# Kernel optimization log

Hardware: AMD Instinct MI355X
Metric: run time of the kernel (lower is better)

The kernel has to match this reference:

```python
import jax, jax.numpy as jnp
import numpy as np

L = 16          # num_sites
CHI_MAX = 64    # max bond dimension
VOCAB = 128000
TRUNC_EVERY = 10
DT = jnp.float32


def _mps_add(A, B):
    """Direct sum of two MPS (block-diagonal on bonds, boundaries concatenated)."""
    out = []
    for s in range(L):
        a, b = A[s], B[s]
        cla, d, cra = a.shape
        clb, _, crb = b.shape
        if s == 0:
            out.append(jnp.concatenate([a, b], axis=2))          # [1,d,cra+crb]
        elif s == L - 1:
            out.append(jnp.concatenate([a, b], axis=0))          # [cla+clb,d,1]
        else:
            t = jnp.zeros((cla + clb, d, cra + crb), a.dtype)
            t = t.at[:cla, :, :cra].set(a).at[cla:, :, cra:].set(b)
            out.append(t)
    return out


def _truncate(T, chi_max):
    """Left-to-right SVD sweep truncating every bond to <= chi_max."""
    T = list(T)
    for s in range(L - 1):
        cl, d, cr = T[s].shape
        U, S, Vh = jnp.linalg.svd(T[s].reshape(cl * d, cr), full_matrices=False)
        k = min(chi_max, int(S.shape[0]))
        T[s] = U[:, :k].reshape(cl, d, k)
        carry = S[:k, None] * Vh[:k]                              # [k, cr]
        T[s + 1] = jnp.einsum('kl,ldr->kdr', carry, T[s + 1])
    return T


def _forward(cores_hidden, cores_input, head_w, head_b, init_ctx, toks):
    # D=1 MPO core -> per-site 2x2 matrix acting on the physical index
    Wh = cores_hidden[:, 0, :, :, 0]   # [L,2,2]
    Wi = cores_input[:, 0, :, :, 0]    # [L,2,2]
    e0 = jnp.array([1.0, 0.0], DT).reshape(1, 2, 1)
    e1 = jnp.array([0.0, 1.0], DT).reshape(1, 2, 1)
    ctx = [init_ctx[s] for s in range(L)]
    for t, tok in enumerate(toks, start=1):
        bits = [(tok >> i) & 1 for i in range(L)]
        emb = [e1 if b else e0 for b in reversed(bits)]
        # h_{t+1} = W_hidden @ h_t  (+)  W_input @ embed(token)
        h = [jnp.einsum('ij,ljr->lir', Wh[s], ctx[s]) for s in range(L)]
        x = [jnp.einsum('ij,ljr->lir', Wi[s], emb[s]) for s in range(L)]
        ctx = _mps_add(h, x)
        if t % TRUNC_EVERY == 0 and ctx[0].shape[2] > CHI_MAX:
            ctx = _truncate(ctx, CHI_MAX)
    # predict(): mean of middle site over (left bond, phys) -> feature vector
    vec = ctx[L // 2].mean(axis=(0, 1))
    c = vec.shape[0]
    vec = jnp.pad(vec, (0, CHI_MAX - c)) if c < CHI_MAX else vec[:CHI_MAX]
    return head_w @ vec + head_b


def setup_inputs() -> dict:
    key = jax.random.key(0)
    k1, k2, k3, k4, k5, k6 = jax.random.split(key, 6)
    eye = jnp.eye(2, dtype=DT)
    cores_hidden = (0.02 * jax.random.normal(k1, (L, 1, 2, 2, 1), DT)).at[:, 0, :, :, 0].add(eye)
    cores_input = (0.02 * jax.random.normal(k2, (L, 1, 2, 2, 1), DT)).at[:, 0, :, :, 0].add(eye)
    head_w = jax.random.normal(k3, (VOCAB, CHI_MAX), DT) / jnp.sqrt(jnp.float32(CHI_MAX))
    head_b = 0.02 * jax.random.normal(k4, (VOCAB,), DT)
    init_ctx = jax.random.normal(k5, (L, 1, 2, 1), DT)
    token_ids = jax.random.randint(k6, (100,), 0, 65536, dtype=jnp.int32)
    return {"cores_hidden": cores_hidden, "cores_input": cores_input,
            "head_w": head_w, "head_b": head_b,
            "init_ctx": init_ctx, "token_ids": token_ids}


def reference(cores_hidden, cores_input, head_w, head_b, init_ctx, token_ids):
    toks = [int(t) for t in np.asarray(token_ids)]
    return _forward(cores_hidden, cores_input, head_w, head_b, init_ctx, toks)
```

## Files before the change

kernel.cpp:

```cpp
#include <hip/hip_runtime.h>

typedef double rl;
#define NT 256
#define NSV 71
#define LDA 128
#define LDV 72
#define SML 25
#define VOCAB 128000
#define LP 27
#define PB 129

#define EPS32 1.1920928955078125e-7
#define UNFL32 1.17549435e-38

#define O_CAR   0
#define O_COLS  4608
#define O_VEC   4800
#define O_MA    5120
#define O_MBLG  14208
#define O_MU    23552
#define O_MQ    32768
#define O_MVT   41984
#define O_SUB   47168
#define O_SVTB  52352
// ... 210 lines not shown
    for(; i<len; ++i) row[(size_t)ld*(1+i)] -= w*(v[(size_t)vstride*i]*scl);
  }
}

__device__ void bdsqr_wave(int n, rl* d, rl* e, int ncvt, int nru, LeafCtx* lc, int lane){
  if(n>1){
    rl eps=EPS32, unfl=UNFL32;
    rl tolmul=fmax(10.0,fmin(100.0,pow(eps,-0.125)));
    rl tol=tolmul*eps;
    rl thresh=0.0;
    int mm=n-1, oldll=-2, oldm=-2, idir=0, iter=0, maxit=6*n*n;
    if(lane==0){
      rl sminoa=fabs(d[0]);
      if(sminoa!=0.0){
        rl mu=sminoa;
        for(int i=1;i<n;++i){ mu=fabs(d[i])*(mu/(mu+fabs(e[i-1]))); sminoa=fmin(sminoa,mu); if(sminoa==0.0)break; }
      }
      sminoa=sminoa/sqrt((rl)n);
      thresh=fmax(tol*sminoa,(rl)(6*n*n)*unfl);
    }
    while(true){
      if(lane==0){
        int act=0, p_lo=0, p_cnt=0, p_fwd=1, p_mm=0;
        while(mm>0){
          if(iter>maxit) break;
          rl smax=fabs(d[mm]), smin=smax;
          int ll=-1;
          for(int lll=mm-1;lll>=0;--lll){
            rl abss=fabs(d[lll]), abse=fabs(e[lll]);
            if(abse<=thresh){ ll=lll; break; }
            smin=fmin(smin,abss);
            smax=fmax(smax,fmax(abss,abse));
          }
          if(ll==mm-1){ e[ll]=0.0; mm=mm-1; continue; }
          if(ll>=0) e[ll]=0.0;
          int lo=ll+1;
          if(mm==lo+1){
            rl sigmn,sigmx,sinr,cosr,sinl,cosl;
            dlasv2(d[lo],e[lo],d[mm],&sigmn,&sigmx,&sinr,&cosr,&sinl,&cosl);
            d[lo]=sigmx; d[mm]=sigmn; e[lo]=0.0;
            lc->sc[0]=cosr; lc->sc[1]=sinr; lc->sc[2]=cosl; lc->sc[3]=sinl;
            act=2; p_lo=lo; p_mm=mm;
            mm-=2;
            break;
          }
          if(lo>oldm || mm<oldll) idir=(fabs(d[lo])>=fabs(d[mm]))?1:2;
          rl sminl=0.0; int conv=0;
          if(idir==1){
            if(fabs(e[mm-1])<=tol*fabs(d[mm])){ e[mm-1]=0.0; conv=1; }
            if(!conv){
              rl mu=fabs(d[lo]); sminl=mu;
              for(int lll=lo;lll<mm;++lll){
                if(fabs(e[lll])<=tol*mu){ e[lll]=0.0; conv=1; break; }
                mu=fabs(d[lll+1])*(mu/(mu+fabs(e[lll])));
                sminl=fmin(sminl,mu);
              }
            }
          } else {
            if(fabs(e[lo])<=tol*fabs(d[lo])){ e[lo]=0.0; conv=1; }
            if(!conv){
              rl mu=fabs(d[mm]); sminl=mu;
              for(int lll=mm-1;lll>=lo;--lll){
                if(fabs(e[lll])<=tol*mu){ e[lll]=0.0; conv=1; break; }
                mu=fabs(d[lll])*(mu/(mu+fabs(e[lll])));
                sminl=fmin(sminl,mu);
              }
            }
          }
          if(conv) continue;
          oldll=lo; oldm=mm;
          rl shift=0.0, rr_;
          if(!((rl)n*tol*(sminl/smax) <= fmax(eps, 0.01*tol))){
            rl sll;
            if(idir==1){ sll=fabs(d[lo]); dlas2(d[mm-1],e[mm-1],d[mm],&shift,&rr_); }
            else { sll=fabs(d[mm]); dlas2(d[lo],e[lo],d[lo+1],&shift,&rr_); }
            if(sll>0.0){ rl q=shift/sll; if(q*q<eps) shift=0.0; }
          }
          iter += mm-lo;
          int cnt=mm-lo;
          if(shift==0.0){
            if(idir==1){
              rl cs=1.0, oldcs=1.0, sn=0.0, oldsn=0.0, r;
              for(int i=lo;i<mm;++i){
                dlartg(d[i]*cs,e[i],&cs,&sn,&r);
                if(i>lo) e[i-1]=oldsn*r;
                dlartg(oldcs*r, d[i+1]*sn, &oldcs,&oldsn,&d[i]);
                lc->b1[i-lo]=cs; lc->b2[i-lo]=sn; lc->b3[i-lo]=oldcs; lc->b4[i-lo]=oldsn;
              }
              rl h=d[mm]*cs; d[mm]=h*oldcs; e[mm-1]=h*oldsn;
              p_fwd=1;
              if(fabs(e[mm-1])<=thresh) e[mm-1]=0.0;
            } else {
              rl cs=1.0, oldcs=1.0, sn=0.0, oldsn=0.0, r;
              for(int i=mm;i>lo;--i){
                dlartg(d[i]*cs,e[i-1],&cs,&sn,&r);
                if(i<mm) e[i]=oldsn*r;
                dlartg(oldcs*r,d[i-1]*sn,&oldcs,&oldsn,&d[i]);
                int j=i-lo-1;
                lc->b1[j]=oldcs; lc->b2[j]=-oldsn; lc->b3[j]=cs; lc->b4[j]=-sn;
              }
              rl h=d[lo]*cs; d[lo]=h*oldcs; e[lo]=h*oldsn;
              p_fwd=0;
              if(fabs(e[lo])<=thresh) e[lo]=0.0;
            }
          } else {
            if(idir==1){
              rl f2=(fabs(d[lo])-shift)*(d_sign(1.0,d[lo])+shift/d[lo]);
              rl g2=e[lo], r, cosr,sinr,cosl,sinl;
              for(int i=lo;i<mm;++i){
                dlartg(f2,g2,&cosr,&sinr,&r);
                if(i>lo) e[i-1]=r;
                f2=cosr*d[i]+sinr*e[i];
                e[i]=cosr*e[i]-sinr*d[i];
                g2=sinr*d[i+1];
                d[i+1]=cosr*d[i+1];
                dlartg(f2,g2,&cosl,&sinl,&r);
                d[i]=r;
                f2=cosl*e[i]+sinl*d[i+1];
                d[i+1]=cosl*d[i+1]-sinl*e[i];
                if(i<mm-1){ g2=sinl*e[i+1]; e[i+1]=cosl*e[i+1]; }
                lc->b1[i-lo]=cosr; lc->b2[i-lo]=sinr; lc->b3[i-lo]=cosl; lc->b4[i-lo]=sinl;
              }
              e[mm-1]=f2;
              p_fwd=1;
              if(fabs(e[mm-1])<=thresh) e[mm-1]=0.0;
            } else {
              rl f2=(fabs(d[mm])-shift)*(d_sign(1.0,d[mm])+shift/d[mm]);
              rl g2=e[mm-1], r, cosr,sinr,cosl,sinl;
              for(int i=mm;i>lo;--i){
                dlartg(f2,g2,&cosr,&sinr,&r);
                if(i<mm) e[i]=r;
                f2=cosr*d[i]+sinr*e[i-1];
                e[i-1]=cosr*e[i-1]-sinr*d[i];
                g2=sinr*d[i-1];
                d[i-1]=cosr*d[i-1];
                dlartg(f2,g2,&cosl,&sinl,&r);
                d[i]=r;
                f2=cosl*e[i-1]+sinl*d[i-1];
                d[i-1]=cosl*d[i-1]-sinl*e[i-1];
                if(i>lo+1){ g2=sinl*e[i-2]; e[i-2]=cosl*e[i-2]; }
                int j=i-lo-1;
                lc->b1[j]=cosl; lc->b2[j]=-sinl; lc->b3[j]=cosr; lc->b4[j]=-sinr;
              }
              e[lo]=f2;
              p_fwd=0;
              if(fabs(e[lo])<=thresh) e[lo]=0.0;
            }
          }
          act=1; p_lo=lo; p_cnt=cnt;
          break;
        }
        lc->si[7]=act; lc->si[8]=p_lo; lc->si[9]=p_cnt; lc->si[10]=p_fwd; lc->si[11]=p_mm;
      }
      wsync();
      int act=lc->si[7];
      if(act==0) break;
      if(act==1){
        int lo=lc->si[8], cnt=lc->si[9], fwd=lc->si[10];
        if(lane<ncvt){
          int k=lane;
          if(fwd){
            rl cur = lc->LVT[lo*LP+k];
            for(int j=0;j<cnt;++j){
              rl c=lc->b1[j], s=lc->b2[j];
              rl t = lc->LVT[(lo+j+1)*LP+k];
              lc->LVT[(lo+j)*LP+k] = s*t + c*cur;
              cur = c*t - s*cur;
            }
            lc->LVT[(lo+cnt)*LP+k] = cur;
          } else {
            rl tcar = lc->LVT[(lo+cnt)*LP+k];
            for(int j=cnt-1;j>=0;--j){
              rl c=lc->b1[j], s=lc->b2[j];
              rl low = lc->LVT[(lo+j)*LP+k];
              lc->LVT[(lo+j+1)*LP+k] = c*tcar - s*low;
              tcar = s*tcar + c*low;
            }
            lc->LVT[lo*LP+k] = tcar;
          }
        } else if(lane<ncvt+nru){
          int r2=lane-ncvt;
          if(fwd){
            rl cur = lc->LU[r2*LP+lo];
            for(int j=0;j<cnt;++j){
              rl c=lc->b3[j], s=lc->b4[j];
              rl t = lc->LU[r2*LP+(lo+j+1)];
              lc->LU[r2*LP+(lo+j)] = s*t + c*cur;
              cur = c*t - s*cur;
            }
            lc->LU[r2*LP+(lo+cnt)] = cur;
          } else {
            rl tcar = lc->LU[r2*LP+(lo+cnt)];
            for(int j=cnt-1;j>=0;--j){
              rl c=lc->b3[j], s=lc->b4[j];
              rl low = lc->LU[r2*LP+(lo+j)];
              lc->LU[r2*LP+(lo+j+1)] = c*tcar - s*low;
              tcar = s*tcar + c*low;
            }
            lc->LU[r2*LP+lo] = tcar;
          }
        }
      } else {
        int lo=lc->si[8], m2=lc->si[11];
        rl cosr=lc->sc[0], sinr=lc->sc[1], cosl=lc->sc[2], sinl=lc->sc[3];
        if(lane<ncvt){
          rl x=lc->LVT[lo*LP+lane], y=lc->LVT[m2*LP+lane];
          lc->LVT[lo*LP+lane]=cosr*x+sinr*y; lc->LVT[m2*LP+lane]=cosr*y-sinr*x;
        } else if(lane<ncvt+nru){
          int r2=lane-ncvt;
          rl x=lc->LU[r2*LP+lo], y=lc->LU[r2*LP+m2];
          lc->LU[r2*LP+lo]=cosl*x+sinl*y; lc->LU[r2*LP+m2]=cosl*y-sinl*x;
        }
      }
      wsync();
    }
  }
  if(lane==0){
    for(int i=0;i<n;++i){ lc->ic[i]=(d[i]<0.0)?1:0; if(d[i]<0.0) d[i]=-d[i]; }
    int nsw=0;
    for(int i=0;i<n-1;++i){
      int isub=0; rl smin=d[0];
      for(int j=1;j<n-i;++j){ if(d[j]<=smin){ isub=j; smin=d[j]; } }
      int tgt=n-1-i;
      if(isub!=tgt){
        d[isub]=d[tgt]; d[tgt]=smin;
        lc->ia[nsw]=isub; lc->ib[nsw]=tgt; ++nsw;
      }
    }
    lc->si[7]=nsw;
  }
  wsync();
  int nsw=lc->si[7];
  if(lane<ncvt){
    for(int i=0;i<n;++i) if(lc->ic[i]) lc->LVT[i*LP+lane]=-lc->LVT[i*LP+lane];
    for(int w2=0;w2<nsw;++w2){
      int a=lc->ia[w2], b=lc->ib[w2];
      rl t=lc->LVT[a*LP+lane]; lc->LVT[a*LP+lane]=lc->LVT[b*LP+lane]; lc->LVT[b*LP+lane]=t;
    }
  } else if(lane<ncvt+nru){
    int r2=lane-ncvt;
    for(int w2=0;w2<nsw;++w2){
      int a=lc->ia[w2], b=lc->ib[w2];
      rl t=lc->LU[r2*LP+a]; lc->LU[r2*LP+a]=lc->LU[r2*LP+b]; lc->LU[r2*LP+b]=t;
    }
  }
  wsync();
}

__device__ void leaf_exec(int f, int n, int sqre, int wantU, LeafCtx* lc, Sh* sh, int lane){
  rl* SVTB = g_ws + O_SVTB; rl* SUB = g_ws + O_SUB;
  int np = n + sqre;
  for(int w=lane; w<np*np; w+=64){ int r2=w/np, c=w-r2*np; lc->LVT[r2*LP+c]=SVTB[(f+r2)+(size_t)LDV*(f+c)]; }
  if(wantU) for(int w=lane; w<n*n; w+=64){ int r2=w/n, c=w-r2*n; lc->LU[r2*LP+c]=SUB[(f+r2)+(size_t)LDV*(f+c)]; }
  wsync();
  if(sqre==1){
    if(lane==0){
      rl cs,snv,rv; rl* dd=sh->d+f; rl* ee=sh->e+f;
      for(int i=0;i<n;++i){
        dlartg(dd[i],ee[i],&cs,&snv,&rv);
        dd[i]=rv;
        if(i<n-1){ ee[i]=snv*dd[i+1]; dd[i+1]=cs*dd[i+1]; }
        else ee[i]=0.0;
        lc->b1[i]=cs; lc->b2[i]=snv;
      }
    }
    wsync();
    if(lane<np){
      rl cur = lc->LVT[0*LP+lane];
      for(int j=0;j<n;++j){
        rl cj=lc->b1[j], sj=lc->b2[j];
        rl t=lc->LVT[(j+1)*LP+lane];
        lc->LVT[j*LP+lane] = sj*t + cj*cur;
        cur = cj*t - sj*cur;
      }
      lc->LVT[n*LP+lane] = cur;
    }
    wsync();
    if(lane==0){
      rl cs,snv,rv; rl* dd=sh->d+f; rl* ee=sh->e+f;
      for(int i=0;i<n-1;++i){
        dlartg(dd[i],ee[i],&cs,&snv,&rv);
        dd[i]=rv; ee[i]=snv*dd[i+1]; dd[i+1]=cs*dd[i+1];
        lc->b1[i]=cs; lc->b2[i]=snv;
      }
    }
    wsync();
    if(wantU && lane<n){
      rl cur = lc->LU[lane*LP+0];
      for(int j=0;j<n-1;++j){
        rl cj=lc->b1[j], sj=lc->b2[j];
        rl t=lc->LU[lane*LP+(j+1)];
        lc->LU[lane*LP+j] = sj*t + cj*cur;
        cur = cj*t - sj*cur;
      }
      lc->LU[lane*LP+(n-1)] = cur;
    }
    wsync();
  }
  bdsqr_wave(n, sh->d+f, sh->e+f, np, wantU? n:0, lc, lane);
  for(int w=lane; w<np*np; w+=64){ int r2=w/np, c=w-r2*np; SVTB[(f+r2)+(size_t)LDV*(f+c)]=lc->LVT[r2*LP+c]; }
  if(wantU) for(int w=lane; w<n*n; w+=64){ int r2=w/n, c=w-r2*n; SUB[(f+r2)+(size_t)LDV*(f+c)]=lc->LU[r2*LP+c]; }
}

__device__ void lasd1_merge(int f, int nl, int nr, int sqre, int wantU, rl* QV, Sh* sh, int tid){
  rl* SUB = g_ws + O_SUB; rl* SVTB = g_ws + O_SVTB;
  rl* U2 = g_ws + O_U2; rl* VT2 = g_ws + O_VT2; rl* QU = g_ws + O_QU;
  int n = nl+nr+1, m = n+sqre;
  if(tid==0){
    rl alpha = sh->d[f+nl], beta = sh->e[f+nl];
    sh->vals[0]=0.0;
    sh->zz[0] = alpha*SVTB[(f+nl)+(size_t)LDV*(f+nl)];
    sh->srcU[0]=-1; sh->srcVT[0]=f+nl;
    for(int i=0;i<nl;++i){
      sh->vals[1+i]=sh->d[f+i];
      sh->zz[1+i]=alpha*SVTB[(f+i)+(size_t)LDV*(f+nl)];
      sh->srcU[1+i]=f+i; sh->srcVT[1+i]=f+i;
    }
    for(int j=0;j<nr;++j){
      sh->vals[1+nl+j]=sh->d[f+nl+1+j];
      sh->zz[1+nl+j]=beta*SVTB[(f+nl+1+j)+(size_t)LDV*(f+nl+1)];
      sh->srcU[1+nl+j]=f+nl+1+j; sh->srcVT[1+nl+j]=f+nl+1+j;
    }
    sh->sc[0]=alpha; sh->sc[1]=beta;
    if(sqre==1){
      rl zM = beta*SVTB[(f+n)+(size_t)LDV*(f+nl+1)];
      rl c,s,r2;
      dlartg(sh->zz[0], zM, &c, &s, &r2);
      sh->zz[0]=r2; sh->sc[2]=c; sh->sc[3]=s;
    }
  }
  __syncthreads();
  if(sqre==1){
    rl c=sh->sc[2], s=sh->sc[3];
    int ra=f+nl, rb=f+n;
    for(int k=tid;k<m;k+=NT){
      size_t ci=(size_t)LDV*(f+k);
      rl a=SVTB[ra+ci], b=SVTB[rb+ci];
      SVTB[ra+ci]=c*a+s*b; SVTB[rb+ci]=-s*a+c*b;
    }
  }
  __syncthreads();
  if(tid==0){
    rl maxd=0.0; for(int i=0;i<n;++i) maxd=fmax(maxd,fabs(sh->vals[i]));
    rl tol = 8.0*EPS32*fmax(maxd, fmax(fabs(sh->sc[0]), fabs(sh->sc[1])));
    int nds=0;
    sh->ic[nds++]=0;
    for(int i=1;i<n;++i) if(fabs(sh->zz[i]) > tol) sh->ic[nds++]=i;
    for(int a=1;a<nds;++a){
      int key=sh->ic[a]; rl kv=sh->vals[key]; int b=a-1;
      while(b>=1 && sh->vals[sh->ic[b]] > kv){ sh->ic[b+1]=sh->ic[b]; --b; }
      sh->ic[b+1]=key;
    }
    int K=nds, pos=nds;
    for(int i=1;i<n;++i) if(fabs(sh->zz[i]) <= tol) sh->ic[pos++]=i;
    for(int a=K+1;a<n;++a){
      int key=sh->ic[a]; rl kv=sh->vals[key]; int b=a-1;
      while(b>=K && sh->vals[sh->ic[b]] > kv){ sh->ic[b+1]=sh->ic[b]; --b; }
      sh->ic[b+1]=key;
    }
    for(int t=0;t<n;++t){ sh->ta[t]=sh->vals[t]; sh->tb[t]=sh->zz[t]; sh->ia[t]=sh->srcU[t]; sh->ib[t]=sh->srcVT[t]; }
    for(int t=0;t<n;++t){
      int p=sh->ic[t];
      sh->dsig[t]=sh->ta[p]; sh->zz[t]=sh->tb[p]; sh->srcU[t]=sh->ia[p]; sh->srcVT[t]=sh->ib[p];
    }
    rl rho=0.0; for(int t=0;t<K;++t){ rl zv=sh->zz[t]; rho += zv*zv; }
    sh->sc[4]=rho;
    sh->si[0]=K; sh->si[1]=n; sh->si[2]=m; sh->si[3]=f; sh->si[4]=nl;
  }
  __syncthreads();
  int K=sh->si[0], n_=sh->si[1], m_=sh->si[2], f_=sh->si[3], nl_=sh->si[4];
  if(wantU){
    for(int w=tid; w<n_*n_; w+=NT){
      int col=w/n_, row=w-col*n_;
      int su=sh->srcU[col];
      rl v;
      if(su<0) v = (row==nl_) ? 1.0 : 0.0;
      else v = SUB[(f_+row)+(size_t)LDV*su];
      U2[row+(size_t)LDV*col]=v;
    }
  }
  for(int w=tid; w<n_*m_; w+=NT){
    int row=w/m_, col=w-row*m_;
    VT2[row+(size_t)LDV*col] = SVTB[sh->srcVT[row]+(size_t)LDV*(f_+col)];
  }
  __syncthreads();
  rl rho=sh->sc[4];
  for(int j=tid;j<K;j+=NT){
    rl lo=sh->dsig[j];
    rl hi=(j<K-1)? sh->dsig[j+1] : sqrt(sh->dsig[K-1]*sh->dsig[K-1]+rho);
    for(int it=0; it<130; ++it){
      rl mid=0.5*(lo+hi);
      if(mid<=lo || mid>=hi) break;
      rl g=1.0;
      for(int i2=0;i2<K;++i2){
        rl zi=sh->zz[i2];
        g += zi*zi/((sh->dsig[i2]-mid)*(sh->dsig[i2]+mid));
      }
      if(g<0.0) lo=mid; else hi=mid;
    }
    sh->sigm[j]=0.5*(lo+hi);
  }
  __syncthreads();
  for(int i2=tid;i2<K;i2+=NT){
    rl di=sh->dsig[i2];
    rl p=(di - sh->sigm[K-1])*(di + sh->sigm[K-1]);
    for(int j=0;j<i2;++j)
      p *= (di - sh->sigm[j])*(di + sh->sigm[j])/((di - sh->dsig[j])*(di + sh->dsig[j]));
    for(int j=i2;j<K-1;++j)
      p *= (di - sh->sigm[j])*(di + sh->sigm[j])/((di - sh->dsig[j+1])*(di + sh->dsig[j+1]));
    sh->zh[i2] = d_sign(sqrt(fabs(p)), sh->zz[i2]);
  }
  __syncthreads();
  for(int j=tid;j<K;j+=NT){
    rl sj=sh->sigm[j];
    rl nu=0.0, nv=0.0;
    for(int i2=0;i2<K;++i2){
      rl di=sh->dsig[i2];
      rl vv=sh->zh[i2]/((di-sj)*(di+sj));
      QV[i2+(size_t)LDV*j]=vv; nv+=vv*vv;
      if(wantU){
        rl uu=(i2==0)? -1.0 : di*vv;
        QU[i2+(size_t)LDV*j]=uu; nu+=uu*uu;
      }
    }
    nv=1.0/sqrt(nv);
    for(int i2=0;i2<K;++i2) QV[i2+(size_t)LDV*j]*=nv;
    if(wantU){
      nu=1.0/sqrt(nu);
      for(int i2=0;i2<K;++i2) QU[i2+(size_t)LDV*j]*=nu;
    }
  }
  __syncthreads();
  if(tid==0){
    int nd2=n_-K;
    for(int t=0;t<nd2;++t) sh->ia[t]=K+t;
    int ps=K-1, pd=nd2-1;
    int t=0;
    while(t<n_){
      rl vs = (ps>=0)? sh->sigm[ps] : -1.0;
      rl vd = (pd>=0)? sh->dsig[sh->ia[pd]] : -1.0;
      if(vs >= vd){ sh->perm[t]=ps; sh->vals[t]=vs; --ps; }
      else { sh->perm[t]=1000+sh->ia[pd]; sh->vals[t]=vd; --pd; }
      ++t;
    }
    for(int q=0;q<n_;++q) sh->d[f_+q]=sh->vals[q];
  }
  __syncthreads();
  if(wantU){
    for(int w=tid; w<n_*n_; w+=NT){
      int t=w/n_, row=w-t*n_;
      int src=sh->perm[t];
      rl acc;
      if(src>=1000) acc = U2[row+(size_t)LDV*(src-1000)];
      else{
        const rl* urow = U2 + row;
        const rl* qcol = QU + (size_t)LDV*src;
        rl s=0.0; int i=0;
        for(; i+16<=K; i+=16){
          rl a[16], b[16];
          #pragma unroll
          for(int u=0;u<16;++u){ a[u]=urow[(size_t)LDV*(size_t)(i+u)]; b[u]=qcol[i+u]; }
          #pragma unroll
          for(int u=0;u<16;++u) s += a[u]*b[u];
        }
        for(; i<K; ++i) s += urow[(size_t)LDV*i]*qcol[i];
        acc=s;
      }
      SUB[(f_+row)+(size_t)LDV*(f_+t)] = acc;
    }
  }
  for(int w=tid; w<n_*m_; w+=NT){
    int t=w/m_, col=w-t*m_;
    int src=sh->perm[t];
    rl acc;
    if(src>=1000) acc = VT2[(src-1000)+(size_t)LDV*col];
    else{
      const rl* qcol = QV + (size_t)LDV*src;
      const rl* vcol = VT2 + (size_t)LDV*col;
      rl s=0.0; int i=0;
      for(; i+16<=K; i+=16){
        rl a[16], b[16];
        #pragma unroll
        for(int u=0;u<16;++u){ a[u]=qcol[i+u]; b[u]=vcol[i+u]; }
        #pragma unroll
        for(int u=0;u<16;++u) s += a[u]*b[u];
      }
      for(; i<K; ++i) s += qcol[i]*vcol[i];
      acc=s;
    }
    SVTB[(f_+t)+(size_t)LDV*(f_+col)] = acc;
  }
  __syncthreads();
}

__device__ void run_dc(int n, int wantU, LeafCtx* lct, Sh* sh, int tid){
  if(tid==0){
    int sf[12], sn2[12], sq[12], sv[12]; int sp=0, no=0;
    sf[0]=0; sn2[0]=n; sq[0]=0; sv[0]=0; sp=1;
    while(sp>0){
      --sp;
      int f=sf[sp], nn=sn2[sp], q=sq[sp], v=sv[sp];
      if(nn<=SML){ sh->opk[no]=0; sh->opf[no]=f; sh->opa[no]=nn; sh->opb[no]=0; sh->opq[no]=q; ++no; }
      else if(v==0){
        int nl=nn/2, nr=nn-nl-1;
        sf[sp]=f; sn2[sp]=nn; sq[sp]=q; sv[sp]=1; ++sp;
        sf[sp]=f+nl+1; sn2[sp]=nr; sq[sp]=q; sv[sp]=0; ++sp;
        sf[sp]=f; sn2[sp]=nl; sq[sp]=1; sv[sp]=0; ++sp;
      } else {
        int nl=nn/2, nr=nn-nl-1;
        sh->opk[no]=1; sh->opf[no]=f; sh->opa[no]=nl; sh->opb[no]=nr; sh->opq[no]=q; ++no;
      }
    }
    int tk[12], tf2[12], ta2[12], tb3[12], tq3[12]; int c=0;
    for(int i=0;i<no;++i) if(sh->opk[i]==0){ tk[c]=0; tf2[c]=sh->opf[i]; ta2[c]=sh->opa[i]; tb3[c]=sh->opb[i]; tq3[c]=sh->opq[i]; ++c; }
    for(int i=0;i<no;++i) if(sh->opk[i]==1){ tk[c]=1; tf2[c]=sh->opf[i]; ta2[c]=sh->opa[i]; tb3[c]=sh->opb[i]; tq3[c]=sh->opq[i]; ++c; }
    for(int i=0;i<no;++i){ sh->opk[i]=tk[i]; sh->opf[i]=tf2[i]; sh->opa[i]=ta2[i]; sh->opb[i]=tb3[i]; sh->opq[i]=tq3[i]; }
    sh->si[6]=no;
  }
  __syncthreads();
  int no=sh->si[6];
  int o=0;
  while(o<no){
    if(sh->opk[o]==0){
      int cnt=1;
      while(o+cnt<no && sh->opk[o+cnt]==0 && cnt<4) ++cnt;
      int wid = tid>>6;
      if(wid<cnt) leaf_exec(sh->opf[o+wid], sh->opa[o+wid], sh->opq[o+wid], wantU, &lct[wid], sh, tid&63);
      __syncthreads();
      o += cnt;
    } else {
      lasd1_merge(sh->opf[o], sh->opa[o], sh->opb[o], sh->opq[o], wantU, (rl*)lct, sh, tid);
      ++o;
    }
  }
}

__device__ void dbdsdc_U(int n, int wantU, LeafCtx* lct, Sh* sh, int tid){
  rl* SUB = g_ws + O_SUB; rl* SVTB = g_ws + O_SVTB;
  for(int w=tid; w<LDV*LDV; w+=NT){
    int c=w/LDV, r2=w-c*LDV; rl v=(r2==c)?1.0:0.0;
    SVTB[w]=v;
    if(wantU) SUB[w]=v;
  }
  __syncthreads();
  if(n <= SML){
    if((tid>>6)==0) leaf_exec(0, n, 0, wantU, &lct[0], sh, tid&63);
    __syncthreads();
  } else run_dc(n, wantU, lct, sh, tid);
}

__device__ void dbdsdc_L(int n, int wantU, LeafCtx* lct, Sh* sh, int tid){
  if(tid==0){
    for(int i=0;i<n-1;++i){
      rl cs,snv,rv;
      dlartg(sh->d[i], sh->e[i], &cs,&snv,&rv);
      sh->d[i]=rv; sh->e[i]=snv*sh->d[i+1]; sh->d[i+1]=cs*sh->d[i+1];
      sh->rc[i]=cs; sh->rs[i]=snv;
    }
  }
  __syncthreads();
  dbdsdc_U(n, wantU, lct, sh, tid);
  if(wantU){
    rl* SUB = g_ws + O_SUB;
    for(int c=tid;c<n;c+=NT){
      size_t ci=(size_t)LDV*c;
      rl carry = SUB[(n-1)+ci];
      for(int k=n-2;k>=0;--k){
        rl a = SUB[k+ci];
        SUB[k+1+ci] = sh->rs[k]*a + sh->rc[k]*carry;
        carry = sh->rc[k]*a - sh->rs[k]*carry;
      }
      SUB[0+ci] = carry;
    }
  }
  __syncthreads();
}

__device__ __forceinline__ void gebd2_upper(rl* A, int ld, int m, int n, Sh* sh, int tid){
  const int lane = tid & 63;
  rl pend_scl = 0.0; int pend_ds = 0;
  for(int i=0;i<n;++i){
    rl ps=0.0;
    for(int r=i+1+lane;r<m;r+=64){ rl vv=A[r+(size_t)ld*i]; ps+=vv*vv; }
    for(int off=32;off>0;off>>=1) ps += __shfl_xor(ps,off,64);
    rl alpha=A[i+(size_t)ld*i];
    rl xn=sqrt(ps);
    rl beta,tau,scl; int ds;
    if(xn==0.0){ tau=0.0; beta=alpha; scl=0.0; ds=0; }
    else{ beta=-d_sign(dlapy2(alpha,xn),alpha); tau=(beta-alpha)/beta; scl=1.0/(alpha-beta); ds=1; }
    if(tid==0){ sh->d[i]=beta; sh->tq[i]=tau; }
    if(tau!=0.0)
      app_left_s(A, ld, i, m, i+1, n, A+(size_t)ld*i, scl, tau, tid);
    if(pend_ds && tid>=128){
      int c = i+1 + (tid-128);
      if(c < n) A[(i-1)+(size_t)ld*c] *= pend_scl;
    }
    __syncthreads();
    if(i<n-1){
      rl ps2=0.0;
      for(int c=i+2+lane;c<n;c+=64){ rl vv=A[i+(size_t)ld*c]; ps2+=vv*vv; }
      for(int off=32;off>0;off>>=1) ps2 += __shfl_xor(ps2,off,64);
      rl alpha2=A[i+(size_t)ld*(i+1)];
      rl xn2=sqrt(ps2);
      rl beta2,tau2,scl2; int ds2;
      if(xn2==0.0){ tau2=0.0; beta2=alpha2; scl2=0.0; ds2=0; }
      else{ beta2=-d_sign(dlapy2(alpha2,xn2),alpha2); tau2=(beta2-alpha2)/beta2; scl2=1.0/(alpha2-beta2); ds2=1; }
      if(tid==0){ sh->e[i]=beta2; sh->tp[i]=tau2; }
      if(tau2!=0.0)
        app_right_s(A, ld, i+1, m, i+1, n, A+i, ld, scl2, tau2, tid);
      if(ds && tid>=128){
        int r = i+1 + (tid-128);
        if(r < m) A[r+(size_t)ld*i] *= scl;
      }
      pend_ds = ds2; pend_scl = scl2;
      __syncthreads();
    } else {
      if(tid==0) sh->tp[i]=0.0;
      __syncthreads();
      if(ds) for(int r=i+1+tid; r<m; r+=NT) A[r+(size_t)ld*(n-1)] *= scl;
      __syncthreads();
    }
  }
}

__device__ __forceinline__ void gebd2_lower(rl* A, int ld, int m, int n, Sh* sh, int tid){
  const int lane = tid & 63;
  rl pend_scl = 0.0; int pend_ds = 0;
  int last_ds = 0; rl last_scl = 0.0;
  for(int i=0;i<m;++i){
    rl ps=0.0;
    for(int c=i+1+lane;c<n;c+=64){ rl vv=A[i+(size_t)ld*c]; ps+=vv*vv; }
    for(int off=32;off>0;off>>=1) ps += __shfl_xor(ps,off,64);
    rl alpha=A[i+(size_t)ld*i];
    rl xn=sqrt(ps);
    rl beta,tau,scl; int ds;
    if(xn==0.0){ tau=0.0; beta=alpha; scl=0.0; ds=0; }
    else{ beta=-d_sign(dlapy2(alpha,xn),alpha); tau=(beta-alpha)/beta; scl=1.0/(alpha-beta); ds=1; }
    if(tid==0){ sh->d[i]=beta; sh->tp[i]=tau; }
    if(tau!=0.0)
      app_right_s(A, ld, i+1, m, i, n, A+i, ld, scl, tau, tid);
    if(pend_ds && tid>=128){
      int r = i+1 + (tid-128);
      if(r < m) A[r+(size_t)ld*(i-1)] *= pend_scl;
    }
    __syncthreads();
    if(i<m-1){
      rl ps2=0.0;
      for(int r=i+2+lane;r<m;r+=64){ rl vv=A[r+(size_t)ld*i]; ps2+=vv*vv; }
      for(int off=32;off>0;off>>=1) ps2 += __shfl_xor(ps2,off,64);
      rl alpha2=A[(i+1)+(size_t)ld*i];
      rl xn2=sqrt(ps2);
      rl beta2,tau2,scl2; int ds2;
      if(xn2==0.0){ tau2=0.0; beta2=alpha2; scl2=0.0; ds2=0; }
      else{ beta2=-d_sign(dlapy2(alpha2,xn2),alpha2); tau2=(beta2-alpha2)/beta2; scl2=1.0/(alpha2-beta2); ds2=1; }
      if(tid==0){ sh->e[i]=beta2; sh->tq[i]=tau2; }
      if(tau2!=0.0)
        app_left_s(A, ld, i+1, m, i+1, n, A+(size_t)ld*i, scl2, tau2, tid);
      if(ds && tid>=128){
        int c = i+1 + (tid-128);
        if(c < n) A[i+(size_t)ld*c] *= scl;
      }
      pend_ds = ds2; pend_scl = scl2;
      __syncthreads();
    } else {
      last_ds = ds; last_scl = scl;
      __syncthreads();
      if(last_ds) for(int c=i+1+tid; c<n; c+=NT) A[(m-1)+(size_t)ld*c] *= last_scl;
      __syncthreads();
    }
  }
}

__device__ __forceinline__ void gelq2(rl* A, int ld, int m, int n, Sh* sh, int tid){
  const int lane = tid & 63;
  rl pend_scl=0.0, pend_beta=0.0; int pend_ds=0;
  for(int i=0;i<m;++i){
    rl ps=0.0;
    for(int c=i+1+lane;c<n;c+=64){ rl vv=A[i+(size_t)ld*c]; ps+=vv*vv; }
    for(int off=32;off>0;off>>=1) ps += __shfl_xor(ps,off,64);
    rl alpha=A[i+(size_t)ld*i];
    rl xn=sqrt(ps);
    rl beta,tau,scl; int ds;
    if(xn==0.0){ tau=0.0; beta=alpha; scl=0.0; ds=0; }
    else{ beta=-d_sign(dlapy2(alpha,xn),alpha); tau=(beta-alpha)/beta; scl=1.0/(alpha-beta); ds=1; }
    if(tid==0) sh->rs[i]=tau;
    if(i<m-1 && tau!=0.0)
      app_right_s(A, ld, i+1, m, i, n, A+i, ld, scl, tau, tid);
    if(i>0 && tid>=128){
      if(pend_ds){ int c = i + (tid-128); if(c<n) A[(i-1)+(size_t)ld*c] *= pend_scl; }
      if(tid==128) A[(i-1)+(size_t)ld*(i-1)] = pend_beta;
    }
    pend_ds=ds; pend_scl=scl; pend_beta=beta;
    __syncthreads();
  }
  if(tid>=128){
    if(pend_ds){ int c = m + (tid-128); if(c<n) A[(m-1)+(size_t)ld*c] *= pend_scl; }
    if(tid==128) A[(m-1)+(size_t)ld*(m-1)] = pend_beta;
  }
  __syncthreads();
}


__global__ __launch_bounds__(NT)
void k_bidiag(const float* __restrict__ ch, const float* __restrict__ ci,
              const float* __restrict__ ictx, const int* __restrict__ tok,
              int s, int m)
{
  __shared__ Sh sh;
  extern __shared__ rl MBL[];
  int tid = threadIdx.x;
  rl* MA = g_ws + O_MA; rl* MQ = g_ws + O_MQ; rl* TB = g_ws + O_TB;
  if(tid==0){
    rl W00=ch[s*4+0], W01=ch[s*4+1], W10=ch[s*4+2], W11=ch[s*4+3];
    rl P00=1,P01=0,P10=0,P11=1;
    for(int mexp=0;mexp<=70;++mexp){
      int j=70-mexp;
      rl v0,v1;
      if(j==0){ v0=ictx[s*2+0]; v1=ictx[s*2+1]; }
      else{
        int b=(tok[j-1]>>(15-s))&1;
        v0=ci[s*4+b]; v1=ci[s*4+2+b];
      }
      g_ws[O_COLS + 0 + 2*j] = P00*v0+P01*v1;
      g_ws[O_COLS + 1 + 2*j] = P10*v0+P11*v1;
      rl n00=W00*P00+W01*P10, n01=W00*P01+W01*P11;
      rl n10=W10*P00+W11*P10, n11=W10*P01+W11*P11;
      P00=n00;P01=n01;P10=n10;P11=n11;
    }
  }
  __syncthreads();
  for(int w=tid; w<m*NSV; w+=NT){
    int j=w/m, r2=w-j*m;
    int l=r2>>1, dd2=r2&1;
    rl cv = g_ws[O_COLS + dd2 + 2*j];
    MA[r2+(size_t)LDA*j] = (s==0)? cv : g_ws[O_CAR + l + 64*j]*cv;
  }
  __syncthreads();
  if(m==128){
    for(int w=tid;w<128*NSV;w+=NT){ int c=w>>7, r2=w&127; MBL[r2+(size_t)PB*c]=MA[r2+(size_t)LDA*c]; }
    __syncthreads();
    gebd2_upper(MBL, PB, 128, NSV, &sh, tid);
    for(int w=tid;w<PB*NSV;w+=NT) g_ws[O_MBLG+w]=MBL[w];
  } else if(m==64){
    for(int w=tid;w<64*NSV;w+=NT){ int c=w>>6, r2=w&63; MBL[r2+(size_t)PB*c]=MA[r2+(size_t)LDA*c]; }
    __syncthreads();
    gebd2_lower(MBL, PB, 64, NSV, &sh, tid);
    for(int w=tid;w<PB*NSV;w+=NT) g_ws[O_MBLG+w]=MBL[w];
  } else {
    for(int w=tid;w<m*NSV;w+=NT){ int c=w/m, r2=w-c*m; MBL[r2+(size_t)PB*c]=MA[r2+(size_t)LDA*c]; }
    __syncthreads();
    gelq2(MBL, PB, m, NSV, &sh, tid);
    for(int w=tid;w<m*NSV;w+=NT){ int c=w/m, r2=w-c*m; MQ[r2+(size_t)LDA*c]=(r2==c)?1.0:0.0; }
    __syncthreads();
    if(tid<m){
      int r=tid;
      for(int j=m-1;j>=0;--j){
        rl tau=sh.rs[j];
        if(tau!=0.0) row_apply(MQ + r + (size_t)LDA*j, LDA, MBL + j + (size_t)PB*(j+1), PB, NSV-j-1, tau);
      }
    }
    __syncthreads();
    for(int w=tid;w<m*m;w+=NT){ int c=w/m, r2=w-c*m; TB[r2+(size_t)LDV*c]=(r2>=c)? MBL[r2+(size_t)PB*c]:0.0; }
    __syncthreads();
    gebd2_upper(TB, LDV, m, m, &sh, tid);
  }
  if(tid<72){
    g_ws[O_D+tid]=sh.d[tid]; g_ws[O_E+tid]=sh.e[tid];
    g_ws[O_TQ+tid]=sh.tq[tid]; g_ws[O_TP+tid]=sh.tp[tid];
  }
}

__global__ __launch_bounds__(NT)
void k_dc(int s, int m)
{
  __shared__ Sh sh;
  __shared__ LeafCtx lct[4];
  int tid = threadIdx.x;
  if(tid<72){ sh.d[tid]=g_ws[O_D+tid]; sh.e[tid]=g_ws[O_E+tid]; }
  __syncthreads();
  int wantU = (s==8)?1:0;
  if(m==128) dbdsdc_U(NSV, wantU, lct, &sh, tid);
  else if(m==64) dbdsdc_L(64, 0, lct, &sh, tid);
  else dbdsdc_U(m, 0, lct, &sh, tid);
  __syncthreads();
  if(tid<72) g_ws[O_D+tid]=sh.d[tid];
}

__global__ __launch_bounds__(NT)
void k_post(const float* __restrict__ ch, int s, int m)
{
  __shared__ Sh sh;
  extern __shared__ rl MBL[];
  int tid = threadIdx.x;
  rl* MU=g_ws+O_MU; rl* MVT=g_ws+O_MVT; rl* MQ=g_ws+O_MQ;
  rl* SUB=g_ws+O_SUB; rl* SVTB=g_ws+O_SVTB; rl* TB=g_ws+O_TB; rl* VT2=g_ws+O_VT2;
  if(tid<72){
    sh.d[tid]=g_ws[O_D+tid];
    sh.tq[tid]=g_ws[O_TQ+tid];
    sh.tp[tid]=g_ws[O_TP+tid];
  }
  __syncthreads();
  int k = (m<64)? m : 64;
  if(m==128){
    if(s==8){
      for(int w=tid;w<128*NSV;w+=NT){ int c=w>>7, r2=w&127; MU[r2+(size_t)LDA*c]=(r2<NSV)? SUB[r2+(size_t)LDV*c]:0.0; }
      for(int w=tid;w<PB*NSV;w+=NT) MBL[w]=g_ws[O_MBLG+w];
      __syncthreads();
      if(tid<NSV){
        int c=tid;
        rl* colb = MU + (size_t)LDA*c;
        for(int i=NSV-1;i>=0;--i){
          rl tau=sh.tq[i];
          if(tau!=0.0) row_apply(colb+i, 1, MBL + (size_t)PB*i + i + 1, 1, 128-i-1, tau);
        }
      }
      __syncthreads();
      if(tid==0){
        rl W00=ch[8*4+0], W01=ch[8*4+1], W10=ch[8*4+2], W11=ch[8*4+3];
        rl P00=1,P01=0,P10=0,P11=1;
        for(int it=0;it<30;++it){
          rl n00=W00*P00+W01*P10, n01=W00*P01+W01*P11;
          rl n10=W10*P00+W11*P10, n11=W10*P01+W11*P11;
          P00=n00;P01=n01;P10=n10;P11=n11;
        }
        sh.sc[0]=P00+P10; sh.sc[1]=P01+P11;
      }
      __syncthreads();
      for(int r2=tid; r2<64; r2+=NT){
        rl acc=0.0;
        for(int l=0;l<64;++l)
          acc += sh.sc[0]*MU[(2*l)+(size_t)LDA*r2] + sh.sc[1]*MU[(2*l+1)+(size_t)LDA*r2];
        g_ws[O_VEC + r2] = acc/188.0;
      }
    } else {
      for(int w=tid;w<LDV*NSV;w+=NT) MVT[w]=SVTB[w];
      for(int w=tid;w<PB*NSV;w+=NT) MBL[w]=g_ws[O_MBLG+w];
      __syncthreads();
      if(tid<NSV){
        int r=tid;
        for(int i=NSV-2;i>=0;--i){
          rl tau=sh.tp[i];
          if(tau!=0.0) row_apply(MVT + r + (size_t)LDV*(i+1), LDV, MBL + i + (size_t)PB*(i+2), PB, NSV-i-2, tau);
        }
      }
      __syncthreads();
      for(int w=tid; w<k*NSV; w+=NT){
        int j=w/k, l=w-j*k;
        g_ws[O_CAR + l + 64*j] = sh.d[l]*MVT[l+(size_t)LDV*j];
      }
    }
  } else if(m==64){
    for(int w=tid;w<64*NSV;w+=NT){ int c=w>>6, r2=w&63; MVT[r2+(size_t)LDV*c]=(c<64)? SVTB[r2+(size_t)LDV*c]:0.0; }
    for(int w=tid;w<PB*NSV;w+=NT) MBL[w]=g_ws[O_MBLG+w];
    __syncthreads();
    if(tid<64){
      int r=tid;
      for(int i=63;i>=0;--i){
        rl tau=sh.tp[i];
        if(tau!=0.0) row_apply(MVT + r + (size_t)LDV*i, LDV, MBL + i + (size_t)PB*(i+1), PB, NSV-i-1, tau);
      }
    }
    __syncthreads();
    for(int w=tid; w<k*NSV; w+=NT){
      int j=w/k, l=w-j*k;
      g_ws[O_CAR + l + 64*j] = sh.d[l]*MVT[l+(size_t)LDV*j];
    }
  } else {
    for(int w=tid;w<m*m;w+=NT){ int c=w/m, r2=w-c*m; VT2[r2+(size_t)LDV*c]=SVTB[r2+(size_t)LDV*c]; }
    __syncthreads();
    if(tid<m){
      int r=tid;
      for(int i=m-2;i>=0;--i){
        rl tau=sh.tp[i];
        if(tau!=0.0) row_apply(VT2 + r + (size_t)LDV*(i+1), LDV, TB + i + (size_t)LDV*(i+2), LDV, m-i-2, tau);
      }
    }
    __syncthreads();
    for(int w=tid;w<m*NSV;w+=NT){
      int c=w/m, r2=w-c*m;
      const rl* vrow = VT2 + r2;
      const rl* qcol = MQ + (size_t)LDA*c;
      rl s2=0.0; int t=0;
      for(; t+16<=m; t+=16){
        rl a[16], b[16];
        #pragma unroll
        for(int u=0;u<16;++u){ a[u]=vrow[(size_t)LDV*(size_t)(t+u)]; b[u]=qcol[t+u]; }
        #pragma unroll
        for(int u=0;u<16;++u) s2 += a[u]*b[u];
      }
      for(; t+4<=m; t+=4){
        rl a0=vrow[(size_t)LDV*t], a1=vrow[(size_t)LDV*(t+1)], a2=vrow[(size_t)LDV*(t+2)], a3=vrow[(size_t)LDV*(t+3)];
        rl b0=qcol[t], b1=qcol[t+1], b2=qcol[t+2], b3=qcol[t+3];
        s2+=a0*b0; s2+=a1*b1; s2+=a2*b2; s2+=a3*b3;
      }
      for(; t<m; ++t) s2 += vrow[(size_t)LDV*t]*qcol[t];
      MVT[r2+(size_t)LDV*c]=s2;
    }
    __syncthreads();
    for(int w=tid; w<k*NSV; w+=NT){
      int j=w/k, l=w-j*k;
      g_ws[O_CAR + l + 64*j] = sh.d[l]*MVT[l+(size_t)LDV*j];
    }
  }
}

__global__ __launch_bounds__(NT)
void head_kernel(const float* __restrict__ hw, const float* __restrict__ hb,
                 float* __restrict__ out)
{
  __shared__ float v[64];
  int tid=threadIdx.x;
  if(tid<64) v[tid]=(float)g_ws[O_VEC + tid];
  __syncthreads();
  int i = blockIdx.x*NT + tid;
  if(i<VOCAB){
    const float4* row = (const float4*)(hw + (size_t)i*64);
    float acc=0.f;
    #pragma unroll
    for(int c4=0;c4<16;++c4){
      float4 r4=row[c4];
      acc += r4.x*v[4*c4] + r4.y*v[4*c4+1] + r4.z*v[4*c4+2] + r4.w*v[4*c4+3];
    }
    out[i]=acc+hb[i];
  }
}

extern "C" void kernel_launch(void* const* d_in, const int* in_sizes, int n_in,
                              void* d_out, int out_size, void* d_ws, size_t ws_size,
                              hipStream_t stream)
{
  const float* ch  = (const float*)d_in[0];
  const float* ci  = (const float*)d_in[1];
  const float* hw  = (const float*)d_in[2];
  const float* hb  = (const float*)d_in[3];
  const float* ict = (const float*)d_in[4];
  const int*   tk  = (const int*)d_in[5];
  (void)d_ws; (void)ws_size; (void)in_sizes; (void)n_in; (void)out_size;

  static const int ms[9] = {2,4,8,16,32,64,128,128,128};
  size_t dynls = (size_t)PB*NSV*sizeof(double);
  for(int s=0;s<9;++s){
    hipLaunchKernelGGL(k_bidiag, dim3(1), dim3(NT), dynls, stream, ch, ci, ict, tk, s, ms[s]);
    hipLaunchKernelGGL(k_dc,     dim3(1), dim3(NT), 0,     stream, s, ms[s]);
    hipLaunchKernelGGL(k_post,   dim3(1), dim3(NT), dynls, stream, ch, s, ms[s]);
  }
  hipLaunchKernelGGL(head_kernel, dim3((VOCAB+NT-1)/NT), dim3(NT), 0, stream,
                     hw, hb, (float*)d_out);
}
```

Baseline: 8.969 ms.

## Split divide-and-conquer SVD into leaf and merge kernels; parallelize merge bookkeeping

Splits the single-block k_dc kernel into k_leaf (leaf bidiagonal SVDs) and k_merge (secular-equation merges), with QV moved into a static LDS array in the merge kernel. Inside lasd1_merge, the serial thread-0 setup, deflation sort (insertion sort) and permutation are replaced by per-thread work: a wave-reduced max and a rank-based parallel sort. The aim is to cut serial single-thread time and register/LDS pressure in the D&C stage. In exchange it adds an extra kernel launch per large step, more __syncthreads, and an O(n^2) rank computation per thread.

```diff
diff --git a/kernel.cpp b/kernel.cpp
--- a/kernel.cpp
+++ b/kernel.cpp
@@ -536,35 +536,67 @@
   if(wantU) for(int w=lane; w<n*n; w+=64){ int r2=w/n, c=w-r2*n; SUB[(f+r2)+(size_t)LDV*(f+c)]=lc->LU[r2*LP+c]; }
 }
 
+__device__ void build_ops(int n, Sh* sh, int tid){
+  if(tid==0){
+    int sf[12], sn2[12], sq[12], sv[12]; int sp=0, no=0;
+    sf[0]=0; sn2[0]=n; sq[0]=0; sv[0]=0; sp=1;
+    while(sp>0){
+      --sp;
+      int f=sf[sp], nn=sn2[sp], q=sq[sp], v=sv[sp];
+      if(nn<=SML){ sh->opk[no]=0; sh->opf[no]=f; sh->opa[no]=nn; sh->opb[no]=0; sh->opq[no]=q; ++no; }
+      else if(v==0){
+        int nl=nn/2, nr=nn-nl-1;
+        sf[sp]=f; sn2[sp]=nn; sq[sp]=q; sv[sp]=1; ++sp;
+        sf[sp]=f+nl+1; sn2[sp]=nr; sq[sp]=q; sv[sp]=0; ++sp;
+        sf[sp]=f; sn2[sp]=nl; sq[sp]=1; sv[sp]=0; ++sp;
+      } else {
+        int nl=nn/2, nr=nn-nl-1;
+        sh->opk[no]=1; sh->opf[no]=f; sh->opa[no]=nl; sh->opb[no]=nr; sh->opq[no]=q; ++no;
+      }
+    }
+    int tk[12], tf2[12], ta2[12], tb3[12], tq3[12]; int c=0;
+    for(int i=0;i<no;++i) if(sh->opk[i]==0){ tk[c]=0; tf2[c]=sh->opf[i]; ta2[c]=sh->opa[i]; tb3[c]=sh->opb[i]; tq3[c]=sh->opq[i]; ++c; }
+    for(int i=0;i<no;++i) if(sh->opk[i]==1){ tk[c]=1; tf2[c]=sh->opf[i]; ta2[c]=sh->opa[i]; tb3[c]=sh->opb[i]; tq3[c]=sh->opq[i]; ++c; }
+    for(int i=0;i<no;++i){ sh->opk[i]=tk[i]; sh->opf[i]=tf2[i]; sh->opa[i]=ta2[i]; sh->opb[i]=tb3[i]; sh->opq[i]=tq3[i]; }
+    sh->si[6]=no;
+  }
+  __syncthreads();
+}
+
 __device__ void lasd1_merge(int f, int nl, int nr, int sqre, int wantU, rl* QV, Sh* sh, int tid){
   rl* SUB = g_ws + O_SUB; rl* SVTB = g_ws + O_SVTB;
   rl* U2 = g_ws + O_U2; rl* VT2 = g_ws + O_VT2; rl* QU = g_ws + O_QU;
   int n = nl+nr+1, m = n+sqre;
-  if(tid==0){
+  {
     rl alpha = sh->d[f+nl], beta = sh->e[f+nl];
-    sh->vals[0]=0.0;
-    sh->zz[0] = alpha*SVTB[(f+nl)+(size_t)LDV*(f+nl)];
-    sh->srcU[0]=-1; sh->srcVT[0]=f+nl;
-    for(int i=0;i<nl;++i){
-      sh->vals[1+i]=sh->d[f+i];
-      sh->zz[1+i]=alpha*SVTB[(f+i)+(size_t)LDV*(f+nl)];
-      sh->srcU[1+i]=f+i; sh->srcVT[1+i]=f+i;
-    }
-    for(int j=0;j<nr;++j){
-      sh->vals[1+nl+j]=sh->d[f+nl+1+j];
-      sh->zz[1+nl+j]=beta*SVTB[(f+nl+1+j)+(size_t)LDV*(f+nl+1)];
-      sh->srcU[1+nl+j]=f+nl+1+j; sh->srcVT[1+nl+j]=f+nl+1+j;
-    }
-    sh->sc[0]=alpha; sh->sc[1]=beta;
-    if(sqre==1){
-      rl zM = beta*SVTB[(f+n)+(size_t)LDV*(f+nl+1)];
-      rl c,s,r2;
-      dlartg(sh->zz[0], zM, &c, &s, &r2);
-      sh->zz[0]=r2; sh->sc[2]=c; sh->sc[3]=s;
+    if(tid==0){
+      sh->sc[0]=alpha; sh->sc[1]=beta;
+      sh->vals[0]=0.0;
+      sh->zz[0] = alpha*SVTB[(f+nl)+(size_t)LDV*(f+nl)];
+      sh->srcU[0]=-1; sh->srcVT[0]=f+nl;
+    } else if(tid<n){
+      int i=tid;
+      if(i<=nl){
+        sh->vals[i]=sh->d[f+i-1];
+        sh->zz[i]=alpha*SVTB[(f+i-1)+(size_t)LDV*(f+nl)];
+        sh->srcU[i]=f+i-1; sh->srcVT[i]=f+i-1;
+      } else {
+        int j=i-1-nl;
+        sh->vals[i]=sh->d[f+nl+1+j];
+        sh->zz[i]=beta*SVTB[(f+nl+1+j)+(size_t)LDV*(f+nl+1)];
+        sh->srcU[i]=f+nl+1+j; sh->srcVT[i]=f+nl+1+j;
+      }
     }
   }
   __syncthreads();
   if(sqre==1){
+    if(tid==0){
+      rl zM = sh->sc[1]*SVTB[(f+n)+(size_t)LDV*(f+nl+1)];
+      rl c,s2,r2;
+      dlartg(sh->zz[0], zM, &c, &s2, &r2);
+      sh->zz[0]=r2; sh->sc[2]=c; sh->sc[3]=s2;
+    }
+    __syncthreads();
     rl c=sh->sc[2], s=sh->sc[3];
     int ra=f+nl, rb=f+n;
     for(int k=tid;k<m;k+=NT){
@@ -574,35 +606,50 @@
     }
   }
   __syncthreads();
+  {
+    rl lm = (tid<n)? fabs(sh->vals[tid]) : 0.0;
+    for(int off=32;off>0;off>>=1) lm = fmax(lm, __shfl_xor(lm,off,64));
+    if((tid&63)==0) sh->ta[tid>>6]=lm;
+  }
+  __syncthreads();
+  {
+    rl maxd = fmax(fmax(sh->ta[0],sh->ta[1]), fmax(sh->ta[2],sh->ta[3]));
+    rl tol = 8.0*EPS32*fmax(maxd, fmax(fabs(sh->sc[0]), fabs(sh->sc[1])));
+    if(tid>=1 && tid<n){
+      bool ndt = fabs(sh->zz[tid])>tol;
+      rl vt = sh->vals[tid];
+      int rank=0, Kc=0;
+      for(int j=1;j<n;++j){
+        bool ndj = fabs(sh->zz[j])>tol;
+        if(ndj) ++Kc;
+        if(ndj==ndt){
+          rl vj=sh->vals[j];
+          if(vj<vt || (vj==vt && j<tid)) ++rank;
+        }
+      }
+      int pos = ndt ? (1+rank) : (1+Kc+rank);
+      sh->ic[pos]=tid;
+    }
+    if(tid==0){
+      int Kc=0;
+      for(int j=1;j<n;++j) if(fabs(sh->zz[j])>tol) ++Kc;
+      sh->ic[0]=0;
+      sh->si[0]=1+Kc; sh->si[1]=n; sh->si[2]=m; sh->si[3]=f; sh->si[4]=nl;
+    }
+  }
+  __syncthreads();
+  int K=sh->si[0], n_=sh->si[1], m_=sh->si[2], f_=sh->si[3], nl_=sh->si[4];
+  if(tid<n_){ sh->ta[tid]=sh->vals[tid]; sh->tb[tid]=sh->zz[tid]; sh->ia[tid]=sh->srcU[tid]; sh->ib[tid]=sh->srcVT[tid]; }
+  __syncthreads();
+  if(tid<n_){
+    int p=sh->ic[tid];
+    sh->dsig[tid]=sh->ta[p]; sh->zz[tid]=sh->tb[p]; sh->srcU[tid]=sh->ia[p]; sh->srcVT[tid]=sh->ib[p];
+  }
+  __syncthreads();
   if(tid==0){
-    rl maxd=0.0; for(int i=0;i<n;++i) maxd=fmax(maxd,fabs(sh->vals[i]));
-    rl tol = 8.0*EPS32*fmax(maxd, fmax(fabs(sh->sc[0]), fabs(sh->sc[1])));
-    int nds=0;
-    sh->ic[nds++]=0;
-    for(int i=1;i<n;++i) if(fabs(sh->zz[i]) > tol) sh->ic[nds++]=i;
-    for(int a=1;a<nds;++a){
-      int key=sh->ic[a]; rl kv=sh->vals[key]; int b=a-1;
-      while(b>=1 && sh->vals[sh->ic[b]] > kv){ sh->ic[b+1]=sh->ic[b]; --b; }
-      sh->ic[b+1]=key;
-    }
-    int K=nds, pos=nds;
-    for(int i=1;i<n;++i) if(fabs(sh->zz[i]) <= tol) sh->ic[pos++]=i;
-    for(int a=K+1;a<n;++a){
-      int key=sh->ic[a]; rl kv=sh->vals[key]; int b=a-1;
-      while(b>=K && sh->vals[sh->ic[b]] > kv){ sh->ic[b+1]=sh->ic[b]; --b; }
-      sh->ic[b+1]=key;
-    }
-    for(int t=0;t<n;++t){ sh->ta[t]=sh->vals[t]; sh->tb[t]=sh->zz[t]; sh->ia[t]=sh->srcU[t]; sh->ib[t]=sh->srcVT[t]; }
-    for(int t=0;t<n;++t){
-      int p=sh->ic[t];
-      sh->dsig[t]=sh->ta[p]; sh->zz[t]=sh->tb[p]; sh->srcU[t]=sh->ia[p]; sh->srcVT[t]=sh->ib[p];
-    }
     rl rho=0.0; for(int t=0;t<K;++t){ rl zv=sh->zz[t]; rho += zv*zv; }
     sh->sc[4]=rho;
-    sh->si[0]=K; sh->si[1]=n; sh->si[2]=m; sh->si[3]=f; sh->si[4]=nl;
-  }
-  __syncthreads();
-  int K=sh->si[0], n_=sh->si[1], m_=sh->si[2], f_=sh->si[3], nl_=sh->si[4];
+  }
   if(wantU){
     for(int w=tid; w<n_*n_; w+=NT){
       int col=w/n_, row=w-col*n_;
@@ -677,9 +724,9 @@
       else { sh->perm[t]=1000+sh->ia[pd]; sh->vals[t]=vd; --pd; }
       ++t;
     }
-    for(int q=0;q<n_;++q) sh->d[f_+q]=sh->vals[q];
-  }
-  __syncthreads();
+  }
+  __syncthreads();
+  if(tid<n_) sh->d[f_+tid]=sh->vals[tid];
   if(wantU){
     for(int w=tid; w<n_*n_; w+=NT){
       int t=w/n_, row=w-t*n_;
@@ -727,89 +774,6 @@
   __syncthreads();
 }
 
-__device__ void run_dc(int n, int wantU, LeafCtx* lct, Sh* sh, int tid){
-  if(tid==0){
-    int sf[12], sn2[12], sq[12], sv[12]; int sp=0, no=0;
-    sf[0]=0; sn2[0]=n; sq[0]=0; sv[0]=0; sp=1;
-    while(sp>0){
-      --sp;
-      int f=sf[sp], nn=sn2[sp], q=sq[sp], v=sv[sp];
-      if(nn<=SML){ sh->opk[no]=0; sh->opf[no]=f; sh->opa[no]=nn; sh->opb[no]=0; sh->opq[no]=q; ++no; }
-      else if(v==0){
-        int nl=nn/2, nr=nn-nl-1;
-        sf[sp]=f; sn2[sp]=nn; sq[sp]=q; sv[sp]=1; ++sp;
-        sf[sp]=f+nl+1; sn2[sp]=nr; sq[sp]=q; sv[sp]=0; ++sp;
-        sf[sp]=f; sn2[sp]=nl; sq[sp]=1; sv[sp]=0; ++sp;
-      } else {
-        int nl=nn/2, nr=nn-nl-1;
-        sh->opk[no]=1; sh->opf[no]=f; sh->opa[no]=nl; sh->opb[no]=nr; sh->opq[no]=q; ++no;
-      }
-    }
-    int tk[12], tf2[12], ta2[12], tb3[12], tq3[12]; int c=0;
-    for(int i=0;i<no;++i) if(sh->opk[i]==0){ tk[c]=0; tf2[c]=sh->opf[i]; ta2[c]=sh->opa[i]; tb3[c]=sh->opb[i]; tq3[c]=sh->opq[i]; ++c; }
-    for(int i=0;i<no;++i) if(sh->opk[i]==1){ tk[c]=1; tf2[c]=sh->opf[i]; ta2[c]=sh->opa[i]; tb3[c]=sh->opb[i]; tq3[c]=sh->opq[i]; ++c; }
-    for(int i=0;i<no;++i){ sh->opk[i]=tk[i]; sh->opf[i]=tf2[i]; sh->opa[i]=ta2[i]; sh->opb[i]=tb3[i]; sh->opq[i]=tq3[i]; }
-    sh->si[6]=no;
-  }
-  __syncthreads();
-  int no=sh->si[6];
-  int o=0;
-  while(o<no){
-    if(sh->opk[o]==0){
-      int cnt=1;
-      while(o+cnt<no && sh->opk[o+cnt]==0 && cnt<4) ++cnt;
-      int wid = tid>>6;
-      if(wid<cnt) leaf_exec(sh->opf[o+wid], sh->opa[o+wid], sh->opq[o+wid], wantU, &lct[wid], sh, tid&63);
-      __syncthreads();
-      o += cnt;
-    } else {
-      lasd1_merge(sh->opf[o], sh->opa[o], sh->opb[o], sh->opq[o], wantU, (rl*)lct, sh, tid);
-      ++o;
-    }
-  }
-}
-
-__device__ void dbdsdc_U(int n, int wantU, LeafCtx* lct, Sh* sh, int tid){
-  rl* SUB = g_ws + O_SUB; rl* SVTB = g_ws + O_SVTB;
-  for(int w=tid; w<LDV*LDV; w+=NT){
-    int c=w/LDV, r2=w-c*LDV; rl v=(r2==c)?1.0:0.0;
-    SVTB[w]=v;
-    if(wantU) SUB[w]=v;
-  }
-  __syncthreads();
-  if(n <= SML){
-    if((tid>>6)==0) leaf_exec(0, n, 0, wantU, &lct[0], sh, tid&63);
-    __syncthreads();
-  } else run_dc(n, wantU, lct, sh, tid);
-}
-
-__device__ void dbdsdc_L(int n, int wantU, LeafCtx* lct, Sh* sh, int tid){
-  if(tid==0){
-    for(int i=0;i<n-1;++i){
-      rl cs,snv,rv;
-      dlartg(sh->d[i], sh->e[i], &cs,&snv,&rv);
-      sh->d[i]=rv; sh->e[i]=snv*sh->d[i+1]; sh->d[i+1]=cs*sh->d[i+1];
-      sh->rc[i]=cs; sh->rs[i]=snv;
-    }
-  }
-  __syncthreads();
-  dbdsdc_U(n, wantU, lct, sh, tid);
-  if(wantU){
-    rl* SUB = g_ws + O_SUB;
-    for(int c=tid;c<n;c+=NT){
-      size_t ci=(size_t)LDV*c;
-      rl carry = SUB[(n-1)+ci];
-      for(int k=n-2;k>=0;--k){
-        rl a = SUB[k+ci];
-        SUB[k+1+ci] = sh->rs[k]*a + sh->rc[k]*carry;
-        carry = sh->rc[k]*a - sh->rs[k]*carry;
-      }
-      SUB[0+ci] = carry;
-    }
-  }
-  __syncthreads();
-}
-
 __device__ __forceinline__ void gebd2_upper(rl* A, int ld, int m, int n, Sh* sh, int tid){
   const int lane = tid & 63;
   rl pend_scl = 0.0; int pend_ds = 0;
@@ -1005,7 +969,7 @@
 }
 
 __global__ __launch_bounds__(NT)
-void k_dc(int s, int m)
+void k_leaf(int s, int m)
 {
   __shared__ Sh sh;
   __shared__ LeafCtx lct[4];
@@ -1013,9 +977,61 @@
   if(tid<72){ sh.d[tid]=g_ws[O_D+tid]; sh.e[tid]=g_ws[O_E+tid]; }
   __syncthreads();
   int wantU = (s==8)?1:0;
-  if(m==128) dbdsdc_U(NSV, wantU, lct, &sh, tid);
-  else if(m==64) dbdsdc_L(64, 0, lct, &sh, tid);
-  else dbdsdc_U(m, 0, lct, &sh, tid);
+  int n_eff = (m==128)? NSV : m;
+  if(m==64){
+    if(tid==0){
+      for(int i=0;i<63;++i){
+        rl cs,snv,rv;
+        dlartg(sh.d[i], sh.e[i], &cs,&snv,&rv);
+        sh.d[i]=rv; sh.e[i]=snv*sh.d[i+1]; sh.d[i+1]=cs*sh.d[i+1];
+      }
+    }
+    __syncthreads();
+  }
+  rl* SUB = g_ws + O_SUB; rl* SVTB = g_ws + O_SVTB;
+  for(int w=tid; w<LDV*LDV; w+=NT){
+    int c=w/LDV, r2=w-c*LDV; rl v=(r2==c)?1.0:0.0;
+    SVTB[w]=v;
+    if(wantU) SUB[w]=v;
+  }
+  __syncthreads();
+  if(n_eff<=SML){
+    if((tid>>6)==0) leaf_exec(0, n_eff, 0, wantU, &lct[0], &sh, tid&63);
+    __syncthreads();
+  } else {
+    build_ops(n_eff, &sh, tid);
+    int no=sh.si[6];
+    int o=0;
+    while(o<no && sh.opk[o]==0){
+      int cnt=1;
+      while(o+cnt<no && sh.opk[o+cnt]==0 && cnt<4) ++cnt;
+      int wid = tid>>6;
+      if(wid<cnt) leaf_exec(sh.opf[o+wid], sh.opa[o+wid], sh.opq[o+wid], wantU, &lct[wid], &sh, tid&63);
+      __syncthreads();
+      o += cnt;
+    }
+  }
+  if(tid<72){ g_ws[O_D+tid]=sh.d[tid]; g_ws[O_E+tid]=sh.e[tid]; }
+}
+
+__global__ __launch_bounds__(NT)
+void k_merge(int s, int m)
+{
+  __shared__ Sh sh;
+  __shared__ rl QV[(size_t)LDV*71];
+  int tid = threadIdx.x;
+  if(tid<72){ sh.d[tid]=g_ws[O_D+tid]; sh.e[tid]=g_ws[O_E+tid]; }
+  __syncthreads();
+  int wantU = (s==8)?1:0;
+  int n_eff = (m==128)? NSV : m;
+  if(n_eff>SML){
+    build_ops(n_eff, &sh, tid);
+    int no=sh.si[6];
+    for(int o=0;o<no;++o){
+      if(sh.opk[o]==1)
+        lasd1_merge(sh.opf[o], sh.opa[o], sh.opb[o], sh.opq[o], wantU, QV, &sh, tid);
+    }
+  }
   __syncthreads();
   if(tid<72) g_ws[O_D+tid]=sh.d[tid];
 }
@@ -1175,7 +1191,9 @@
   size_t dynls = (size_t)PB*NSV*sizeof(double);
   for(int s=0;s<9;++s){
     hipLaunchKernelGGL(k_bidiag, dim3(1), dim3(NT), dynls, stream, ch, ci, ict, tk, s, ms[s]);
-    hipLaunchKernelGGL(k_dc,     dim3(1), dim3(NT), 0,     stream, s, ms[s]);
+    hipLaunchKernelGGL(k_leaf,   dim3(1), dim3(NT), 0,     stream, s, ms[s]);
+    if(ms[s] >= 32)
+      hipLaunchKernelGGL(k_merge, dim3(1), dim3(NT), 0,    stream, s, ms[s]);
     hipLaunchKernelGGL(k_post,   dim3(1), dim3(NT), dynls, stream, ch, s, ms[s]);
   }
   hipLaunchKernelGGL(head_kernel, dim3((VOCAB+NT-1)/NT), dim3(NT), 0, stream,
```

New measurement: 8.123 ms. -9.4%, faster.
